# Kernel tuning notes

Hardware: AMD Instinct MI355X
Metric: run time of the kernel (lower is better)

Reference implementation:

```python
import jax, jax.numpy as jnp
import numpy as np

NEG = -1e30  # stand-in for -inf that keeps logsumexp/grads NaN-free


def setup_inputs() -> dict:
    key = jax.random.key(0)
    k1, k2, k3 = jax.random.split(key, 3)
    B, T, V, L = 32, 1024, 1000, 128
    pred = jax.random.normal(k1, (B, T, V), dtype=jnp.float32)
    # labels avoid the blank index 0
    target = jax.random.randint(k2, (B, L), 1, V)
    target_length = jax.random.randint(k3, (B,), L // 2, L + 1)
    return {"pred": pred, "target": target, "target_length": target_length, "batch_size": B}


def _wctc_neg_log_lik(log_probs, targets, target_lengths, blank):
    """W-CTC (wildcard CTC, ICLR'22): CTC forward DP with a wildcard state
    prepended and appended to the extended label sequence. The wildcard emits
    any frame with probability 1 (log-prob 0), so alignments may start late
    and end early.  log_probs: (T,B,V) log-softmaxed; targets: (B,L).
    Returns per-sample negative log-likelihood, shape (B,)."""
    T, B, V = log_probs.shape
    L = targets.shape[1]
    S = 2 * L + 2  # s=0 start-star, odd s blank, even s>=2 label (s-2)//2; end-star kept as a separate scalar state
    s = jnp.arange(S)
    is_star = s == 0
    is_blank = s % 2 == 1
    lab = jnp.clip((s - 2) // 2, 0, L - 1)
    prev_lab = jnp.clip((s - 4) // 2, 0, L - 1)
    tok = jnp.where((is_blank | is_star)[None, :], blank, targets[:, lab])  # (B,S)
    same = targets[:, lab] == targets[:, prev_lab]
    # skip transition s-2 -> s allowed for label states whose label differs from
    # the previous label (s==2 skips from the start-star, always allowed)
    skip = (~is_blank)[None, :] & (~is_star)[None, :] & ((s == 2)[None, :] | ~same)  # (B,S)
    # states beyond the true extended sequence (per-sample target length) are invalid
    valid = s[None, :] <= (2 * target_lengths + 1)[:, None]  # (B,S)
    bidx = jnp.arange(B)
    ll = 2 * target_lengths       # index of last label state
    lb = ll + 1                   # index of last blank state

    def emit(lp_t):  # (B,V) -> (B,S); star emits with log-prob 0
        e = jnp.take_along_axis(lp_t, tok, axis=1)
        return jnp.where(is_star[None, :], 0.0, e)

    e0 = emit(log_probs[0])
    alpha0 = jnp.full((B, S), NEG, dtype=log_probs.dtype)
    alpha0 = alpha0.at[:, 0].set(0.0).at[:, 1].set(e0[:, 1]).at[:, 2].set(e0[:, 2])
    alpha0 = jnp.where(valid, alpha0, NEG)
    endstar0 = jnp.full((B,), NEG, dtype=log_probs.dtype)

    def step(carry, lp_t):
        alpha, endstar = carry
        # end-star absorbs from last blank / last label, emission log-prob 0
        endstar = jax.nn.logsumexp(
            jnp.stack([endstar, alpha[bidx, ll], alpha[bidx, lb]]), axis=0)
        p1 = jnp.concatenate([jnp.full((B, 1), NEG, alpha.dtype), alpha[:, :-1]], axis=1)
        p2 = jnp.concatenate([jnp.full((B, 2), NEG, alpha.dtype), alpha[:, :-2]], axis=1)
        p2 = jnp.where(skip, p2, NEG)
        alpha = emit(lp_t) + jax.nn.logsumexp(jnp.stack([alpha, p1, p2]), axis=0)
        alpha = jnp.where(valid, alpha, NEG)
        return (alpha, endstar), None

    (alpha, endstar), _ = jax.lax.scan(step, (alpha0, endstar0), log_probs[1:])
    total = jax.nn.logsumexp(
        jnp.stack([alpha[bidx, ll], alpha[bidx, lb], endstar]), axis=0)
    return -total


def reference(pred, target, target_length, batch_size):
    # pred: (B,T,V) raw logits -> log_softmax over vocab, then time-major
    lp = jax.nn.log_softmax(pred, axis=-1)
    lp = jnp.transpose(lp, (1, 0, 2))  # (T,B,V)
    nll = _wctc_neg_log_lik(lp, target, target_length, blank=0)  # (B,)
    # torch CTC 'mean' reduction: divide by target length, then batch mean
    return jnp.mean(nll / target_length.astype(nll.dtype))
```

## Files before the change

kernel.cpp:

```cpp
#include <hip/hip_runtime.h>

#define LOG2E 1.4426950408889634f
#define LN2   0.6931471805599453f

__device__ __forceinline__ float x2(float x)  { return __builtin_amdgcn_exp2f(x); }
__device__ __forceinline__ float lg2(float x) { return __builtin_amdgcn_logf(x); }

__device__ __forceinline__ float dpp_shr1_f(float x) {
    return __int_as_float(
        __builtin_amdgcn_update_dpp(0, __float_as_int(x), 0x138, 0xf, 0xf, false));
}
__device__ __forceinline__ int dpp_shr1_i(int x) {
    return __builtin_amdgcn_update_dpp(0, x, 0x138, 0xf, 0xf, false);
}

#define GLLDS(g, l, sz)                                                    \
    __builtin_amdgcn_global_load_lds(                                      \
        (const __attribute__((address_space(1))) void*)(g),                \
        (__attribute__((address_space(3))) void*)(l), (sz), 0, 0)

__global__ __launch_bounds__(256) void emit_kernel(const float* __restrict__ pred,
                                                   const int* __restrict__ target,
                                                   float* __restrict__ emA,
                                                   float* __restrict__ emB,
                                                   int T, int V, int L) {
    int wave = threadIdx.x >> 6;
    int lane = threadIdx.x & 63;
    int row = blockIdx.x * 4 + wave;
    const float* rowp = pred + (size_t)row * V;
    int nq = V >> 2;
    float4 v0, v1, v2, v3;
    const float4 fill = make_float4(-3.0e38f, -3.0e38f, -3.0e38f, -3.0e38f);
    v0 = (lane       < nq) ? ((const float4*)rowp)[lane]       : fill;
    v1 = (lane + 64  < nq) ? ((const float4*)rowp)[lane + 64]  : fill;
    v2 = (lane + 128 < nq) ? ((const float4*)rowp)[lane + 128] : fill;
    v3 = (lane + 192 < nq) ? ((const float4*)rowp)[lane + 192] : fill;
    float lm = fmaxf(fmaxf(fmaxf(v0.x, v0.y), fmaxf(v0.z, v0.w)),
               fmaxf(fmaxf(fmaxf(v1.x, v1.y), fmaxf(v1.z, v1.w)),
               fmaxf(fmaxf(fmaxf(v2.x, v2.y), fmaxf(v2.z, v2.w)),
                     fmaxf(fmaxf(v3.x, v3.y), fmaxf(v3.z, v3.w)))));
    #pragma unroll
    for (int off = 32; off > 0; off >>= 1) lm = fmaxf(lm, __shfl_xor(lm, off));
    float mm = lm * LOG2E;
    float ls = 0.f;
    if (lane < nq)
        ls += x2(fmaf(v0.x, LOG2E, -mm)) + x2(fmaf(v0.y, LOG2E, -mm))
            + x2(fmaf(v0.z, LOG2E, -mm)) + x2(fmaf(v0.w, LOG2E, -mm));
    if (lane + 64 < nq)
        ls += x2(fmaf(v1.x, LOG2E, -mm)) + x2(fmaf(v1.y, LOG2E, -mm))
            + x2(fmaf(v1.z, LOG2E, -mm)) + x2(fmaf(v1.w, LOG2E, -mm));
    if (lane + 128 < nq)
        ls += x2(fmaf(v2.x, LOG2E, -mm)) + x2(fmaf(v2.y, LOG2E, -mm))
            + x2(fmaf(v2.z, LOG2E, -mm)) + x2(fmaf(v2.w, LOG2E, -mm));
    if (lane + 192 < nq)
        ls += x2(fmaf(v3.x, LOG2E, -mm)) + x2(fmaf(v3.y, LOG2E, -mm))
            + x2(fmaf(v3.z, LOG2E, -mm)) + x2(fmaf(v3.w, LOG2E, -mm));
    #pragma unroll
    for (int off = 32; off > 0; off >>= 1) ls += __shfl_xor(ls, off);
    float n2 = mm + lg2(ls);

    int b = row / T;
    int t = row - b * T;
    int p = t >> 1, par = t & 1;
    const int* tg = target + b * L;
    float* arow = emA + ((size_t)b * (T >> 1) + p) * 256;
    for (int j = lane; j < L; j += 64) {
        int tok = tg[j];
        arow[(j >> 1) * 4 + par * 2 + (j & 1)] = x2(fmaf(rowp[tok], LOG2E, -n2));
    }
    float blank_logit = __shfl(v0.x, 0);
    if (lane == 0) emB[row] = x2(fmaf(blank_logit, LOG2E, -n2));
}

#define STEP_CORE(EX0, EX1, EB)                                           \
  do {                                                                    \
    float r  = a3 + a2;                                                   \
    float q  = a1 + a0;                                                   \
    float w  = skipAn ? r : a3;        \
    float ur = dpp_shr1_f(w);                                             \
    int   Kp = dpp_shr1_i(K);                                             \
    K = act ? K : Kp;                                                     \
    float uc = ldexpf(ur, K - Kp);                                        \
    float sb = s1 + star_st;                                              \
    if (lane == 0) uc = sb;                                               \
    S += slot0 ? q : r;                                                   \
    a2 = (EX1) * (a2 + (skipB ? q : a1));                                 \
    a0 = (EX0) * (a0 + uc);                                               \
    a1 = (EB) * q;                                                        \
    a3 = (EB) * r;                                                        \
    s1 = (EB) * sb;                                                       \
    act = act || (uc > 0.0f);                                             \
  } while (0)

#define RENORM                                                            \
  do {                                                                    \
    float m4 = fmaxf(fmaxf(a0, a1), fmaxf(a2, a3));                       \
    int e = (int)((__float_as_uint(m4) >> 23) & 255u) - 127;              \
    int d = act ? -e : 0;                                                 \
    float sc = ldexpf(1.0f, d);                                           \
    a0 *= sc; a1 *= sc; a2 *= sc; a3 *= sc; s1 *= sc; S *= sc;            \
    K += d;                                                               \
    star_st = ldexpf(sbase, K);                                           \
  } while (0)

#define BATCH 24

__global__ __launch_bounds__(64, 1) void dp_kernel(const float* __restrict__ emA,
                                                   const float* __restrict__ emB,
                                                   const int* __restrict__ target,
                                                   const int* __restrict__ tlen,
                                                   float* __restrict__ nll,
                                                   int T, int L) {
    __shared__ float4 sA[2][BATCH][64];
    __shared__ float  sB[2][64];

    int b = blockIdx.x;
    int lane = threadIdx.x;
    int NP = T >> 1;
    int NPm1 = NP - 1;
    const float* eAb = emA + (size_t)b * NP * 256;
    const float* eBb = emB + (size_t)b * T;
    const int* tg = target + b * L;

    int NPc = NP - 1;
    int NB = (NPc + BATCH - 1) / BATCH;

    #define ISSUE(c, buf)                                                  \
      do {                                                                 \
        int base_ = 1 + BATCH * (c);                                       \
        _Pragma("unroll")                                                  \
        for (int j_ = 0; j_ < BATCH; ++j_) {                               \
            int pr_ = base_ + j_; if (pr_ > NPm1) pr_ = NPm1;              \
            GLLDS(eAb + (size_t)pr_ * 256, &sA[buf][j_][0], 16);           \
        }                                                                  \
        GLLDS(eBb + base_ * 2, &sB[buf][0], 4);                            \
      } while (0)

    ISSUE(0, 0);
    if (NB > 1) ISSUE(1, 1);

    float4 p0 = ((const float4*)eAb)[lane];
    float be0 = eBb[0], be1 = eBb[1];

    int t0 = tg[2 * lane];
    int t1 = tg[2 * lane + 1];
    int tprev = __shfl_up(t1, 1);
    bool skipA = (lane == 0) || (t0 != tprev);
    bool skipAn = (__shfl_down((int)skipA, 1) != 0);
    bool skipB = (t1 != t0);

    int tl = tlen[b];
    int ll = 2 * tl;
    int lane_e = (ll - 2) >> 2;
    bool slot0 = ((ll - 2) & 3) == 0;

    float a0 = (lane == 0) ? p0.x : 0.f;
    float a1 = 0.f, a2 = 0.f, a3 = 0.f;
    float s1 = (lane == 0) ? be0 : 0.f;
    float sbase = (lane == 0) ? 1.0f : 0.0f;
    int   K = 0;
    float star_st = sbase;
    bool  act = (lane == 0);
    float S = 0.f;

    STEP_CORE(p0.z, p0.w, be1);

    for (int c = 0; c < NB; ++c) {
        asm volatile("s_waitcnt vmcnt(0)" ::: "memory");
        int buf = c & 1;
        int jn = NPc - BATCH * c; if (jn > BATCH) jn = BATCH;
        float4 e0 = sA[buf][0][lane];
        float2 h0 = *(const float2*)&sB[buf][0];
        float4 e1 = sA[buf][1][lane];
        float2 h1 = *(const float2*)&sB[buf][2];
        for (int j = 0; j < jn; ++j) {
            int j2 = j + 2; if (j2 >= BATCH) j2 -= BATCH;
            float4 e2 = sA[buf][j2][lane];
            float2 h2 = *(const float2*)&sB[buf][2 * j2];
            STEP_CORE(e0.x, e0.y, h0.x);
            STEP_CORE(e0.z, e0.w, h0.y);
            if (j & 1) RENORM;
            e0 = e1; h0 = h1;
            e1 = e2; h1 = h2;
        }
        if (c + 2 < NB) ISSUE(c + 2, buf);
    }
    #undef ISSUE

    {
        float q = a1 + a0;
        float r = a3 + a2;
        S += slot0 ? q : r;
    }
    float Sv = __shfl(S, lane_e);
    int   Kv = __shfl(K, lane_e);
    if (lane == 0) nll[b] = -((lg2(Sv) - (float)Kv) * LN2);
}

__global__ __launch_bounds__(64) void fin_kernel(const float* __restrict__ nll,
                                                 const int* __restrict__ tlen,
                                                 float* __restrict__ out, int B) {
    int tid = threadIdx.x;
    float v = (tid < B) ? nll[tid] / (float)tlen[tid] : 0.f;
    #pragma unroll
    for (int off = 32; off > 0; off >>= 1) v += __shfl_xor(v, off);
    if (tid == 0) out[0] = v / (float)B;
}

extern "C" void kernel_launch(void* const* d_in, const int* in_sizes, int n_in,
                              void* d_out, int out_size, void* d_ws, size_t ws_size,
                              hipStream_t stream) {
    const float* pred   = (const float*)d_in[0];
    const int*   target = (const int*)d_in[1];
    const int*   tlen   = (const int*)d_in[2];
    int B = in_sizes[2];
    int L = in_sizes[1] / B;
    int V = 1000;
    int T = in_sizes[0] / (B * V);

    float* ws  = (float*)d_ws;
    float* nll = ws;
    float* emB = ws + 64;
    float* emA = emB + (size_t)B * T;

    emit_kernel<<<(B * T) / 4, 256, 0, stream>>>(pred, target, emA, emB, T, V, L);
    dp_kernel<<<B, 64, 0, stream>>>(emA, emB, target, tlen, nll, T, L);
    fin_kernel<<<1, 64, 0, stream>>>(nll, tlen, (float*)d_out, B);
}
```

Baseline: 295.9 us.

## Interleave two batch samples' DP recurrences per wavefront with partial load waits

Each dp_kernel wavefront now advances the forward recurrences of two batch samples at once. Their independent step sequences are interleaved so that dependent VALU/DPP latency in one chain can overlap with work from the other. The prefetch wait is relaxed from vmcnt(0) to vmcnt(26), so only the older LDS batch must land while the newer one stays in flight, and the batch size is halved to fit the doubled shared buffers. The grid shrinks to half as many blocks, and extra clamped prefetches are issued past the end of the data.

```diff
diff --git a/kernel.cpp b/kernel.cpp
--- a/kernel.cpp
+++ b/kernel.cpp
@@ -72,58 +72,84 @@
     if (lane == 0) emB[row] = x2(fmaf(blank_logit, LOG2E, -n2));
 }
 
-#define STEP_CORE(EX0, EX1, EB)                                           \
-  do {                                                                    \
-    float r  = a3 + a2;                                                   \
-    float q  = a1 + a0;                                                   \
-    float w  = skipAn ? r : a3;        \
-    float ur = dpp_shr1_f(w);                                             \
-    int   Kp = dpp_shr1_i(K);                                             \
-    K = act ? K : Kp;                                                     \
-    float uc = ldexpf(ur, K - Kp);                                        \
-    float sb = s1 + star_st;                                              \
-    if (lane == 0) uc = sb;                                               \
-    S += slot0 ? q : r;                                                   \
-    a2 = (EX1) * (a2 + (skipB ? q : a1));                                 \
-    a0 = (EX0) * (a0 + uc);                                               \
-    a1 = (EB) * q;                                                        \
-    a3 = (EB) * r;                                                        \
-    s1 = (EB) * sb;                                                       \
-    act = act || (uc > 0.0f);                                             \
-  } while (0)
-
-#define RENORM                                                            \
-  do {                                                                    \
-    float m4 = fmaxf(fmaxf(a0, a1), fmaxf(a2, a3));                       \
-    int e = (int)((__float_as_uint(m4) >> 23) & 255u) - 127;              \
-    int d = act ? -e : 0;                                                 \
-    float sc = ldexpf(1.0f, d);                                           \
-    a0 *= sc; a1 *= sc; a2 *= sc; a3 *= sc; s1 *= sc; S *= sc;            \
-    K += d;                                                               \
-    star_st = ldexpf(sbase, K);                                           \
-  } while (0)
-
-#define BATCH 24
+struct DP {
+    float a0, a1, a2, a3;
+    float s1;
+    float star_st;
+    float S;
+    float sbase;
+    int   K;
+    bool  act;
+    bool  skipAn;
+    bool  skipB;
+    bool  slot0;
+    int   lane_e;
+};
+
+__device__ __forceinline__ void dp_step(DP& d, float ex0, float ex1, float eb,
+                                        int lane) {
+    float r  = d.a3 + d.a2;
+    float q  = d.a1 + d.a0;
+    float w  = d.skipAn ? r : d.a3;
+    float ur = dpp_shr1_f(w);
+    int   Kp = dpp_shr1_i(d.K);
+    d.K = d.act ? d.K : Kp;
+    float uc = ldexpf(ur, d.K - Kp);
+    float sb = d.s1 + d.star_st;
+    if (lane == 0) uc = sb;
+    d.S += d.slot0 ? q : r;
+    d.a2 = ex1 * (d.a2 + (d.skipB ? q : d.a1));
+    d.a0 = ex0 * (d.a0 + uc);
+    d.a1 = eb * q;
+    d.a3 = eb * r;
+    d.s1 = eb * sb;
+    d.act = d.act || (uc > 0.0f);
+}
+
+__device__ __forceinline__ void dp_renorm(DP& d) {
+    float m4 = fmaxf(fmaxf(d.a0, d.a1), fmaxf(d.a2, d.a3));
+    int e = (int)((__float_as_uint(m4) >> 23) & 255u) - 127;
+    int dd = d.act ? -e : 0;
+    float sc = ldexpf(1.0f, dd);
+    d.a0 *= sc; d.a1 *= sc; d.a2 *= sc; d.a3 *= sc; d.s1 *= sc; d.S *= sc;
+    d.K += dd;
+    d.star_st = ldexpf(d.sbase, d.K);
+}
+
+#define BATCH 12
 
 __global__ __launch_bounds__(64, 1) void dp_kernel(const float* __restrict__ emA,
                                                    const float* __restrict__ emB,
                                                    const int* __restrict__ target,
                                                    const int* __restrict__ tlen,
                                                    float* __restrict__ nll,
-                                                   int T, int L) {
-    __shared__ float4 sA[2][BATCH][64];
-    __shared__ float  sB[2][64];
-
-    int b = blockIdx.x;
+                                                   int T, int L, int B) {
+    __shared__ float4 sA[2][2][BATCH][64];
+    __shared__ float  sB[2][2][64];
+
     int lane = threadIdx.x;
+    int b0 = blockIdx.x * 2;
+    int b1i = b0 + 1;
+    int b1 = (b1i < B) ? b1i : b0;
     int NP = T >> 1;
     int NPm1 = NP - 1;
-    const float* eAb = emA + (size_t)b * NP * 256;
-    const float* eBb = emB + (size_t)b * T;
-    const int* tg = target + b * L;
+    const float* eA0 = emA + (size_t)b0 * NP * 256;
+    const float* eA1 = emA + (size_t)b1 * NP * 256;
+    const float* eB0 = emB + (size_t)b0 * T;
+    const float* eB1 = emB + (size_t)b1 * T;
+    const int* tg0 = target + b0 * L;
+    const int* tg1 = target + b1 * L;
 
     int NPc = NP - 1;
     int NB = (NPc + BATCH - 1) / BATCH;
+
+    float4 p0a = ((const float4*)eA0)[lane];
+    float4 p0b = ((const float4*)eA1)[lane];
+    float be0a = eB0[0], be1a = eB0[1];
+    float be0b = eB1[0], be1b = eB1[1];
+    int t0a = tg0[2 * lane], t1a = tg0[2 * lane + 1];
+    int t0b = tg1[2 * lane], t1b = tg1[2 * lane + 1];
+    int tla = tlen[b0], tlb = tlen[b1];
 
     #define ISSUE(c, buf)                                                  \
       do {                                                                 \
@@ -131,70 +157,92 @@
         _Pragma("unroll")                                                  \
         for (int j_ = 0; j_ < BATCH; ++j_) {                               \
             int pr_ = base_ + j_; if (pr_ > NPm1) pr_ = NPm1;              \
-            GLLDS(eAb + (size_t)pr_ * 256, &sA[buf][j_][0], 16);           \
+            GLLDS(eA0 + (size_t)pr_ * 256, &sA[buf][0][j_][0], 16);        \
+            GLLDS(eA1 + (size_t)pr_ * 256, &sA[buf][1][j_][0], 16);        \
         }                                                                  \
-        GLLDS(eBb + base_ * 2, &sB[buf][0], 4);                            \
+        int bb_ = base_ * 2; if (bb_ > T - 1) bb_ = T - 1;                 \
+        GLLDS(eB0 + bb_, &sB[buf][0][0], 4);                               \
+        GLLDS(eB1 + bb_, &sB[buf][1][0], 4);                               \
       } while (0)
 
     ISSUE(0, 0);
-    if (NB > 1) ISSUE(1, 1);
-
-    float4 p0 = ((const float4*)eAb)[lane];
-    float be0 = eBb[0], be1 = eBb[1];
-
-    int t0 = tg[2 * lane];
-    int t1 = tg[2 * lane + 1];
-    int tprev = __shfl_up(t1, 1);
-    bool skipA = (lane == 0) || (t0 != tprev);
-    bool skipAn = (__shfl_down((int)skipA, 1) != 0);
-    bool skipB = (t1 != t0);
-
-    int tl = tlen[b];
-    int ll = 2 * tl;
-    int lane_e = (ll - 2) >> 2;
-    bool slot0 = ((ll - 2) & 3) == 0;
-
-    float a0 = (lane == 0) ? p0.x : 0.f;
-    float a1 = 0.f, a2 = 0.f, a3 = 0.f;
-    float s1 = (lane == 0) ? be0 : 0.f;
-    float sbase = (lane == 0) ? 1.0f : 0.0f;
-    int   K = 0;
-    float star_st = sbase;
-    bool  act = (lane == 0);
-    float S = 0.f;
-
-    STEP_CORE(p0.z, p0.w, be1);
+    ISSUE(1, 1);
+
+    DP d0, d1;
+    {
+        int tprev = __shfl_up(t1a, 1);
+        bool skipA = (lane == 0) || (t0a != tprev);
+        d0.skipAn = (__shfl_down((int)skipA, 1) != 0);
+        d0.skipB = (t1a != t0a);
+        int ll = 2 * tla;
+        d0.lane_e = (ll - 2) >> 2;
+        d0.slot0 = ((ll - 2) & 3) == 0;
+        d0.a0 = (lane == 0) ? p0a.x : 0.f;
+        d0.a1 = 0.f; d0.a2 = 0.f; d0.a3 = 0.f;
+        d0.s1 = (lane == 0) ? be0a : 0.f;
+        d0.sbase = (lane == 0) ? 1.0f : 0.0f;
+        d0.K = 0; d0.star_st = d0.sbase; d0.act = (lane == 0); d0.S = 0.f;
+    }
+    {
+        int tprev = __shfl_up(t1b, 1);
+        bool skipA = (lane == 0) || (t0b != tprev);
+        d1.skipAn = (__shfl_down((int)skipA, 1) != 0);
+        d1.skipB = (t1b != t0b);
+        int ll = 2 * tlb;
+        d1.lane_e = (ll - 2) >> 2;
+        d1.slot0 = ((ll - 2) & 3) == 0;
+        d1.a0 = (lane == 0) ? p0b.x : 0.f;
+        d1.a1 = 0.f; d1.a2 = 0.f; d1.a3 = 0.f;
+        d1.s1 = (lane == 0) ? be0b : 0.f;
+        d1.sbase = (lane == 0) ? 1.0f : 0.0f;
+        d1.K = 0; d1.star_st = d1.sbase; d1.act = (lane == 0); d1.S = 0.f;
+    }
+
+    dp_step(d0, p0a.z, p0a.w, be1a, lane);
+    dp_step(d1, p0b.z, p0b.w, be1b, lane);
 
     for (int c = 0; c < NB; ++c) {
-        asm volatile("s_waitcnt vmcnt(0)" ::: "memory");
+        asm volatile("s_waitcnt vmcnt(26)" ::: "memory");
         int buf = c & 1;
         int jn = NPc - BATCH * c; if (jn > BATCH) jn = BATCH;
-        float4 e0 = sA[buf][0][lane];
-        float2 h0 = *(const float2*)&sB[buf][0];
-        float4 e1 = sA[buf][1][lane];
-        float2 h1 = *(const float2*)&sB[buf][2];
+        float4 e0a = sA[buf][0][0][lane], e0b = sA[buf][1][0][lane];
+        float2 h0a = *(const float2*)&sB[buf][0][0];
+        float2 h0b = *(const float2*)&sB[buf][1][0];
+        float4 e1a = sA[buf][0][1][lane], e1b = sA[buf][1][1][lane];
+        float2 h1a = *(const float2*)&sB[buf][0][2];
+        float2 h1b = *(const float2*)&sB[buf][1][2];
         for (int j = 0; j < jn; ++j) {
             int j2 = j + 2; if (j2 >= BATCH) j2 -= BATCH;
-            float4 e2 = sA[buf][j2][lane];
-            float2 h2 = *(const float2*)&sB[buf][2 * j2];
-            STEP_CORE(e0.x, e0.y, h0.x);
-            STEP_CORE(e0.z, e0.w, h0.y);
-            if (j & 1) RENORM;
-            e0 = e1; h0 = h1;
-            e1 = e2; h1 = h2;
+            float4 e2a = sA[buf][0][j2][lane], e2b = sA[buf][1][j2][lane];
+            float2 h2a = *(const float2*)&sB[buf][0][2 * j2];
+            float2 h2b = *(const float2*)&sB[buf][1][2 * j2];
+            dp_step(d0, e0a.x, e0a.y, h0a.x, lane);
+            dp_step(d1, e0b.x, e0b.y, h0b.x, lane);
+            dp_step(d0, e0a.z, e0a.w, h0a.y, lane);
+            dp_step(d1, e0b.z, e0b.w, h0b.y, lane);
+            if (j & 1) { dp_renorm(d0); dp_renorm(d1); }
+            e0a = e1a; h0a = h1a; e1a = e2a; h1a = h2a;
+            e0b = e1b; h0b = h1b; e1b = e2b; h1b = h2b;
         }
-        if (c + 2 < NB) ISSUE(c + 2, buf);
+        ISSUE(c + 2, buf);
     }
     #undef ISSUE
+    asm volatile("s_waitcnt vmcnt(0)" ::: "memory");
 
     {
-        float q = a1 + a0;
-        float r = a3 + a2;
-        S += slot0 ? q : r;
-    }
-    float Sv = __shfl(S, lane_e);
-    int   Kv = __shfl(K, lane_e);
-    if (lane == 0) nll[b] = -((lg2(Sv) - (float)Kv) * LN2);
+        float q = d0.a1 + d0.a0, r = d0.a3 + d0.a2;
+        d0.S += d0.slot0 ? q : r;
+        q = d1.a1 + d1.a0; r = d1.a3 + d1.a2;
+        d1.S += d1.slot0 ? q : r;
+    }
+    float Sv0 = __shfl(d0.S, d0.lane_e);
+    int   Kv0 = __shfl(d0.K, d0.lane_e);
+    float Sv1 = __shfl(d1.S, d1.lane_e);
+    int   Kv1 = __shfl(d1.K, d1.lane_e);
+    if (lane == 0) {
+        nll[b0] = -((lg2(Sv0) - (float)Kv0) * LN2);
+        if (b1i < B) nll[b1i] = -((lg2(Sv1) - (float)Kv1) * LN2);
+    }
 }
 
 __global__ __launch_bounds__(64) void fin_kernel(const float* __restrict__ nll,
@@ -224,6 +272,6 @@
     float* emA = emB + (size_t)B * T;
 
     emit_kernel<<<(B * T) / 4, 256, 0, stream>>>(pred, target, emA, emB, T, V, L);
-    dp_kernel<<<B, 64, 0, stream>>>(emA, emB, target, tlen, nll, T, L);
+    dp_kernel<<<(B + 1) / 2, 64, 0, stream>>>(emA, emB, target, tlen, nll, T, L, B);
     fin_kernel<<<1, 64, 0, stream>>>(nll, tlen, (float*)d_out, B);
 }
```

Result: slower. 363.4 us (+22.8%).

## Fully unroll DP chunk loop and relax vmcnt wait to keep next batch in flight

Applied to the files above, without the earlier changes.

Splits the time-pair loop into full BATCH-sized chunks that are fully unrolled, plus a separate tail loop, replacing the rolling register prefetch of LDS rows. The wait at each chunk now uses a partial vmcnt so the loads for the following chunk can stay outstanding while the current one is consumed, and the issue of chunk c+2 becomes unconditional with a clamped emB index. The aim is less loop overhead and less stalling on global-to-LDS loads along the serial DP critical path. The hard-coded vmcnt(25) assumes a specific count of outstanding loads per chunk, so correctness depends on BATCH matching that value, and unconditional issues may fetch redundant clamped data.

```diff
diff --git a/kernel.cpp b/kernel.cpp
--- a/kernel.cpp
+++ b/kernel.cpp
@@ -123,7 +123,8 @@
     const int* tg = target + b * L;
 
     int NPc = NP - 1;
-    int NB = (NPc + BATCH - 1) / BATCH;
+    int full = NPc / BATCH;
+    int tail = NPc % BATCH;
 
     #define ISSUE(c, buf)                                                  \
       do {                                                                 \
@@ -133,11 +134,12 @@
             int pr_ = base_ + j_; if (pr_ > NPm1) pr_ = NPm1;              \
             GLLDS(eAb + (size_t)pr_ * 256, &sA[buf][j_][0], 16);           \
         }                                                                  \
-        GLLDS(eBb + base_ * 2, &sB[buf][0], 4);                            \
+        int bb_ = base_ * 2; if (bb_ > T - 1) bb_ = T - 1;                 \
+        GLLDS(eBb + bb_, &sB[buf][0], 4);                                  \
       } while (0)
 
     ISSUE(0, 0);
-    if (NB > 1) ISSUE(1, 1);
+    ISSUE(1, 1);
 
     float4 p0 = ((const float4*)eAb)[lane];
     float be0 = eBb[0], be1 = eBb[1];
@@ -165,27 +167,34 @@
 
     STEP_CORE(p0.z, p0.w, be1);
 
-    for (int c = 0; c < NB; ++c) {
+    for (int c = 0; c < full; ++c) {
+        asm volatile("s_waitcnt vmcnt(25)" ::: "memory");
+        int buf = c & 1;
+        const float4 (*sAb)[64] = sA[buf];
+        const float* sBb = sB[buf];
+        #pragma unroll
+        for (int j = 0; j < BATCH; ++j) {
+            float4 e4 = sAb[j][lane];
+            float2 b2 = *(const float2*)&sBb[2 * j];
+            STEP_CORE(e4.x, e4.y, b2.x);
+            STEP_CORE(e4.z, e4.w, b2.y);
+            if (j & 1) RENORM;
+        }
+        ISSUE(c + 2, buf);
+    }
+    if (tail) {
         asm volatile("s_waitcnt vmcnt(0)" ::: "memory");
-        int buf = c & 1;
-        int jn = NPc - BATCH * c; if (jn > BATCH) jn = BATCH;
-        float4 e0 = sA[buf][0][lane];
-        float2 h0 = *(const float2*)&sB[buf][0];
-        float4 e1 = sA[buf][1][lane];
-        float2 h1 = *(const float2*)&sB[buf][2];
-        for (int j = 0; j < jn; ++j) {
-            int j2 = j + 2; if (j2 >= BATCH) j2 -= BATCH;
-            float4 e2 = sA[buf][j2][lane];
-            float2 h2 = *(const float2*)&sB[buf][2 * j2];
-            STEP_CORE(e0.x, e0.y, h0.x);
-            STEP_CORE(e0.z, e0.w, h0.y);
+        int buf = full & 1;
+        for (int j = 0; j < tail; ++j) {
+            float4 e4 = sA[buf][j][lane];
+            float2 b2 = *(const float2*)&sB[buf][2 * j];
+            STEP_CORE(e4.x, e4.y, b2.x);
+            STEP_CORE(e4.z, e4.w, b2.y);
             if (j & 1) RENORM;
-            e0 = e1; h0 = h1;
-            e1 = e2; h1 = h2;
         }
-        if (c + 2 < NB) ISSUE(c + 2, buf);
     }
     #undef ISSUE
+    asm volatile("s_waitcnt vmcnt(0)" ::: "memory");
 
     {
         float q = a1 + a0;
```

Result: faster. 264.8 us (-10.5%).
